# Performance work log

Measured on AMD Instinct MI355X. Metric: run time of the kernel, lower is better.

## Reference

```python
import jax, jax.numpy as jnp
import numpy as np

B, S, D = 4, 2048, 1024
LN_EPS = 1e-5
NEG_INF = -1e9


def _layernorm(x, gamma, beta):
    mu = jnp.mean(x, axis=-1, keepdims=True)
    var = jnp.var(x, axis=-1, keepdims=True)
    return (x - mu) * jax.lax.rsqrt(var + LN_EPS) * gamma + beta


def setup_inputs() -> dict:
    key = jax.random.key(0)
    k1, k2, k3, k4 = jax.random.split(key, 4)
    context = jax.random.normal(k1, (B, S, D), dtype=jnp.float32)
    eos_mask = jnp.ones((B, S, S), dtype=jnp.int64)
    prior = jax.random.uniform(k2, (B, S, S), dtype=jnp.float32)
    bound = 1.0 / np.sqrt(D)
    Wq = jax.random.uniform(k3, (D, D), dtype=jnp.float32, minval=-bound, maxval=bound)
    Wk = jax.random.uniform(k4, (D, D), dtype=jnp.float32, minval=-bound, maxval=bound)
    gamma = jnp.ones((D,), dtype=jnp.float32)
    beta = jnp.zeros((D,), dtype=jnp.float32)
    return {"context": context, "eos_mask": eos_mask, "prior": prior,
            "Wq": Wq, "Wk": Wk, "gamma": gamma, "beta": beta}


def reference(context, eos_mask, prior, Wq, Wk, gamma, beta):
    d_model = context.shape[-1]
    seq_len = context.shape[1]
    x = _layernorm(context, gamma, beta)
    q = x @ Wq.T                                   # nn.Linear, no bias
    k = x @ Wk.T
    scores = jnp.einsum('bsd,btd->bst', q, k) / jnp.sqrt(jnp.asarray(d_model, x.dtype))

    idx = jnp.arange(seq_len)
    a_sup = idx[:, None] + 1 == idx[None, :]       # superdiagonal (torch `a`)
    c_sub = idx[:, None] - 1 == idx[None, :]       # subdiagonal  (torch `c`)
    diag = idx[:, None] == idx[None, :]            # identity     (torch `b`)
    strict_lower = idx[:, None] > idx[None, :]     # tril - eye

    # mask = eos_mask & (a + c)  (Python precedence: & binds looser than +)
    mask = (eos_mask != 0) & (a_sup | c_sub)
    scores = jnp.where(mask, scores, NEG_INF)
    neibor_attn = jax.nn.softmax(scores, axis=-1)
    neibor_attn = jnp.sqrt(neibor_attn * jnp.swapaxes(neibor_attn, -1, -2) + 1e-9)
    neibor_attn = prior + (1.0 - prior) * neibor_attn

    # t = log(neibor+1e-9).masked_fill(a==0,0) @ tril  == reverse cumsum over last axis
    logn = jnp.where(a_sup, jnp.log(neibor_attn + 1e-9), 0.0)
    t = jnp.cumsum(logn[:, :, ::-1], axis=-1)[:, :, ::-1]
    # g = exp(tril @ t), keep strictly-lower part ((tril - eye) != 0)
    g = jnp.exp(jnp.cumsum(t, axis=1))
    g = jnp.where(strict_lower, g, 0.0)

    g_attn = g + jnp.swapaxes(g, -1, -2) + jnp.where(diag, neibor_attn, 1e-9)
    return g_attn, neibor_attn
```

## Files before the change

kernel.cpp:

```cpp
#include <hip/hip_runtime.h>
#include <hip/hip_bf16.h>
#include <stdint.h>

#define SS 2048
#define DD 1024
#define RR 8192

typedef _Float16 f16;
typedef _Float16 f16x8 __attribute__((ext_vector_type(8)));
typedef _Float16 f16x4 __attribute__((ext_vector_type(4)));
typedef float    f32x4 __attribute__((ext_vector_type(4)));

__device__ __forceinline__ void gl_lds16(const f16* g, f16* l) {
  __builtin_amdgcn_global_load_lds((const __attribute__((address_space(1))) void*)g,
                                   (__attribute__((address_space(3))) void*)l,
                                   16, 0, 0);
}

__global__ __launch_bounds__(256) void k_pre(const float* __restrict__ x,
                                             const float* __restrict__ gamma,
                                             const float* __restrict__ beta,
                                             f16* __restrict__ xn,
                                             const float* __restrict__ Wq,
                                             const float* __restrict__ Wk,
                                             f16* __restrict__ Wqt,
                                             f16* __restrict__ Wkt,
                                             const int* __restrict__ eos,
                                             const float* __restrict__ prior,
                                             float* __restrict__ sup_g,
                                             float* __restrict__ sub_g,
                                             int* __restrict__ e_sup,
                                             int* __restrict__ e_sub,
                                             float* __restrict__ pr_sup) {
  __shared__ f16 tile[64][72];
  int bidx = blockIdx.x;
  int t = threadIdx.x;
  if (bidx < RR) {
    int lane = t & 63, w = t >> 6;
    const float* xr = x + (size_t)bidx * DD;
    float4 v = ((const float4*)xr)[t];
    float s  = v.x + v.y + v.z + v.w;
    float ss = v.x*v.x + v.y*v.y + v.z*v.z + v.w*v.w;
#pragma unroll
    for (int off = 32; off > 0; off >>= 1) {
      s  += __shfl_down(s,  off, 64);
      ss += __shfl_down(ss, off, 64);
    }
    float* r0 = (float*)&tile[0][0];
    float* r1 = r0 + 4;
    if (lane == 0) { r0[w] = s; r1[w] = ss; }
    __syncthreads();
    float tot = r0[0]+r0[1]+r0[2]+r0[3];
    float tss = r1[0]+r1[1]+r1[2]+r1[3];
    float mu  = tot * (1.0f/DD);
    float var = tss * (1.0f/DD) - mu*mu;
    float inv = rsqrtf(var + 1e-5f);
    float4 g = ((const float4*)gamma)[t];
    float4 b = ((const float4*)beta)[t];
    f16x4 o;
    o[0] = (f16)((v.x-mu)*inv*g.x + b.x);
    o[1] = (f16)((v.y-mu)*inv*g.y + b.y);
    o[2] = (f16)((v.z-mu)*inv*g.z + b.z);
    o[3] = (f16)((v.w-mu)*inv*g.w + b.w);
    *(f16x4*)(xn + (size_t)bidx*DD + t*4) = o;
  } else if (bidx < RR + 512) {
    int bid = bidx - RR;
    const float* src = (bid & 1) ? Wk : Wq;
    f16* dst = (bid & 1) ? Wkt : Wqt;
    int tb = bid >> 1;
    int r0 = (tb >> 4) << 6, c0 = (tb & 15) << 6;
#pragma unroll
    for (int p = 0; p < 4; ++p) {
      int r = p * 16 + (t >> 4);
      int c = (t & 15) * 4;
      float4 v = *(const float4*)(src + (size_t)(r0 + r) * DD + c0 + c);
      tile[c + 0][r] = (f16)v.x; tile[c + 1][r] = (f16)v.y;
      tile[c + 2][r] = (f16)v.z; tile[c + 3][r] = (f16)v.w;
    }
    __syncthreads();
    int orow = t >> 2, och = (t & 3) * 16;
    f16x8 a = *(const f16x8*)&tile[orow][och];
    f16x8 b = *(const f16x8*)&tile[orow][och + 8];
    f16* o = dst + (size_t)(c0 + orow) * DD + r0 + och;
    *(f16x8*)o = a;
    *(f16x8*)(o + 8) = b;
  } else {
    int g = bidx - (RR + 512);
    int u = g * 256 + t;
    sup_g[u] = 0.f;
    sub_g[u] = 0.f;
    if (u < 4 * 2047) {
      int b = u / 2047;
      int s = u - b * 2047;
      size_t ebase = (size_t)b * SS * SS;
      int bS = b * SS;
      e_sup[bS + s]     = eos[ebase + (size_t)s * SS + s + 1];
      e_sub[bS + s + 1] = eos[ebase + (size_t)(s + 1) * SS + s];
      pr_sup[bS + s]    = prior[ebase + (size_t)s * SS + s + 1];
    }
  }
}

__global__ __launch_bounds__(256) void k_mgemm(const f16* __restrict__ A,
                                               const f16* __restrict__ Bw,
                                               f16* __restrict__ C) {
  constexpr int K = 1024;
  __shared__ f16 As[2][64 * 32];
  __shared__ f16 Bs[2][64 * 32];
  int cpx = (int)gridDim.x >> 3;
  int bid = ((int)blockIdx.x & 7) * cpx + ((int)blockIdx.x >> 3);
  int bm = bid >> 4, bn = bid & 15;
  int tid = threadIdx.x;
  int lane = tid & 63, w = tid >> 6;
  int wm = w >> 1, wn = w & 1;
  f32x4 acc[2][2] = {};

  int srow = w * 16 + (lane >> 2);
  int sch  = lane & 3;
  const f16* Ag = A  + (size_t)(bm * 64 + srow) * K + sch * 8;
  const f16* Bg = Bw + (size_t)(bn * 64 + srow) * K + sch * 8;
  f16* lA = &As[0][0] + w * 16 * 32;
  f16* lB = &Bs[0][0] + w * 16 * 32;
  int rlo = lane & 15, rch = (lane >> 4) * 8;

  gl_lds16(Ag, lA);
  gl_lds16(Bg, lB);
  for (int t = 0; t < 32; ++t) {
    int cur = t & 1;
    __syncthreads();
    if (t < 31) {
      gl_lds16(Ag + (t + 1) * 32, lA + (cur ^ 1) * 64 * 32);
      gl_lds16(Bg + (t + 1) * 32, lB + (cur ^ 1) * 64 * 32);
    }
    f16x8 af[2], bf[2];
#pragma unroll
    for (int mi = 0; mi < 2; ++mi)
      af[mi] = *(const f16x8*)(&As[cur][(wm * 32 + mi * 16 + rlo) * 32 + rch]);
#pragma unroll
    for (int ni = 0; ni < 2; ++ni)
      bf[ni] = *(const f16x8*)(&Bs[cur][(wn * 32 + ni * 16 + rlo) * 32 + rch]);
#pragma unroll
    for (int mi = 0; mi < 2; ++mi)
#pragma unroll
      for (int ni = 0; ni < 2; ++ni)
        acc[mi][ni] = __builtin_amdgcn_mfma_f32_16x16x32_f16(af[mi], bf[ni], acc[mi][ni], 0, 0, 0);
  }
  int c0 = (lane >> 4) * 4;
#pragma unroll
  for (int mi = 0; mi < 2; ++mi)
#pragma unroll
    for (int ni = 0; ni < 2; ++ni)
#pragma unroll
      for (int r = 0; r < 4; ++r) {
        int row = bm * 64 + wm * 32 + mi * 16 + c0 + r;
        int col = bn * 64 + wn * 32 + ni * 16 + rlo;
        C[(size_t)row * DD + col] = (f16)acc[mi][ni][r];
      }
}

__global__ __launch_bounds__(256) void k_ygemm(const f16* __restrict__ A,
                                               const f16* __restrict__ Bw,
                                               float* __restrict__ sup_g,
                                               float* __restrict__ sub_g) {
  constexpr int K = 1024, BM = 128, BN = 128;
  constexpr int XST = 136;
  __shared__ f16 As[BM * 32];
  __shared__ f16 Bs[BN * 32];
  __shared__ f16 Xs[130 * XST];
  int cpx = (int)gridDim.x >> 3;
  int bid = ((int)blockIdx.x & 7) * cpx + ((int)blockIdx.x >> 3);
  int bm = bid >> 3, bn = bid & 7;
  int tid = threadIdx.x;
  int lane = tid & 63, w = tid >> 6;
  int wm = w >> 1, wn = w & 1;

  f32x4 acc[4][4] = {};

  int srow = w * 16 + (lane >> 2);
  int sch  = lane & 3;
  const f16* Ag0 = A  + (size_t)(bm * BM + srow) * K + sch * 8;
  const f16* Ag1 = Ag0 + (size_t)64 * K;
  const f16* Bg0 = Bw + (size_t)(bn * BN + srow) * K + sch * 8;
  const f16* Bg1 = Bg0 + (size_t)64 * K;
  f16* lA0 = As + (w * 16) * 32;
  f16* lA1 = As + (64 + w * 16) * 32;
  f16* lB0 = Bs + (w * 16) * 32;
  f16* lB1 = Bs + (64 + w * 16) * 32;
  int rlo = lane & 15, rch = (lane >> 4) * 8;

  for (int kt = 0; kt < K; kt += 32) {
    __syncthreads();
    gl_lds16(Ag0 + kt, lA0);
    gl_lds16(Ag1 + kt, lA1);
    gl_lds16(Bg0 + kt, lB0);
    gl_lds16(Bg1 + kt, lB1);
    __syncthreads();
    f16x8 af[4], bf[4];
#pragma unroll
    for (int mi = 0; mi < 4; ++mi)
      af[mi] = *(const f16x8*)(As + (wm * 64 + mi * 16 + rlo) * 32 + rch);
#pragma unroll
    for (int ni = 0; ni < 4; ++ni)
      bf[ni] = *(const f16x8*)(Bs + (wn * 64 + ni * 16 + rlo) * 32 + rch);
#pragma unroll
    for (int mi = 0; mi < 4; ++mi)
#pragma unroll
      for (int ni = 0; ni < 4; ++ni)
        acc[mi][ni] = __builtin_amdgcn_mfma_f32_16x16x32_f16(af[mi], bf[ni], acc[mi][ni], 0, 0, 0);
  }
  int c0 = (lane >> 4) * 4;
  int slabBase = bm * BM - 1;
#pragma unroll
  for (int it = 0; it < 9; ++it) {
    int c = tid + it * 256;
    if (c < 130 * 16) {
      int rI = c >> 4, colc = (c & 15) * 8;
      int gr = slabBase + rI;
      gr = gr < 0 ? 0 : (gr > RR - 1 ? RR - 1 : gr);
      *(f16x8*)(Xs + rI * XST + colc) =
          *(const f16x8*)(A + (size_t)gr * K + bn * BN + colc);
    }
  }
  __syncthreads();
#pragma unroll
  for (int mi = 0; mi < 4; ++mi) {
#pragma unroll
    for (int r = 0; r < 4; ++r) {
      int rloc = wm * 64 + mi * 16 + c0 + r;
      float su = 0.f, sb = 0.f;
#pragma unroll
      for (int ni = 0; ni < 4; ++ni) {
        float y = acc[mi][ni][r];
        int colL = wn * 64 + ni * 16 + rlo;
        su += y * (float)Xs[rloc * XST + colL];
        sb += y * (float)Xs[(rloc + 2) * XST + colL];
      }
#pragma unroll
      for (int m = 1; m < 16; m <<= 1) {
        su += __shfl_xor(su, m, 64);
        sb += __shfl_xor(sb, m, 64);
      }
      if (rlo == 0) {
        int rho = bm * BM + rloc;
        if ((rho & (SS - 1)) != 0)
          atomicAdd(&sup_g[rho - 1], su * 0.03125f);
        if ((rho & (SS - 1)) != SS - 1)
          atomicAdd(&sub_g[rho + 1], sb * 0.03125f);
      }
    }
  }
}

__global__ __launch_bounds__(1024) void k_scan(const float* __restrict__ sup,
                                               const float* __restrict__ sub,
                                               const int* __restrict__ e_sup,
                                               const int* __restrict__ e_sub,
                                               const float* __restrict__ pr_sup,
                                               float* __restrict__ p_sup,
                                               float* __restrict__ p_sub,
                                               double* __restrict__ P) {
  int b = blockIdx.x, t = threadIdx.x;
  int lane = t & 63, wid = t >> 6;
  int bS = b * SS;
  __shared__ float  psub_sh[SS];
  __shared__ double wsum[16];
  float psup_loc[2];
#pragma unroll
  for (int e = 0; e < 2; ++e) {
    int s = 2*t + e;
    bool supOK = (s < SS-1) && (e_sup[bS + s] != 0);
    bool subOK = (s >= 1)   && (e_sub[bS + s] != 0);
    float ps = 0.f, pb = 0.f;
    if (supOK && subOK) {
      float Av = sup[bS + s], Cv = sub[bS + s];
      float m  = fmaxf(Av, Cv);
      float ea = expf(Av - m), eb = expf(Cv - m);
      float iv = 1.0f / (ea + eb);
      ps = ea * iv; pb = eb * iv;
    } else if (supOK) ps = 1.f;
    else if (subOK)   pb = 1.f;
    p_sup[bS + s] = ps; p_sub[bS + s] = pb;
    psub_sh[s] = pb; psup_loc[e] = ps;
  }
  __syncthreads();
  double L0 = 0.0, L1 = 0.0;
#pragma unroll
  for (int e = 0; e < 2; ++e) {
    int s = 2*t + e;
    double Lv = 0.0;
    if (s < SS-1) {
      float pr = pr_sup[bS + s];
      float vv = sqrtf(psup_loc[e] * psub_sh[s+1] + 1e-9f);
      Lv = (double)logf(pr + (1.f - pr)*vv + 1e-9f);
    }
    if (e == 0) L0 = Lv; else L1 = Lv;
  }
  double pairv = L0 + L1;
  double v = pairv;
#pragma unroll
  for (int off = 1; off < 64; off <<= 1) {
    double u = __shfl_up(v, off, 64);
    if (lane >= off) v += u;
  }
  if (lane == 63) wsum[wid] = v;
  __syncthreads();
  double base = 0.0;
  for (int wI = 0; wI < wid; ++wI) base += wsum[wI];
  double excl = base + v - pairv;
  P[bS + 2*t]     = excl + L0;
  P[bS + 2*t + 1] = excl + L0 + L1;
}

__global__ __launch_bounds__(256) void k_out(const float* __restrict__ prior,
                                             const float* __restrict__ p_sup,
                                             const float* __restrict__ p_sub,
                                             const double* __restrict__ P,
                                             float* __restrict__ g_out,
                                             float* __restrict__ n_out) {
  size_t v = (size_t)blockIdx.x * 256 + threadIdx.x;
  int j4   = (int)(v & 511);
  int rowg = (int)(v >> 9);
  int s = rowg & (SS - 1);
  int b = rowg >> 11;
  size_t base = (size_t)rowg * SS + j4 * 4;
  union F4 { float4 v4; float a[4]; };
  F4 prf; prf.v4 = *(const float4*)(prior + base);
  int bS = b * SS;
  double Ps  = P[bS + s];
  double Ps2 = (s >= 2) ? P[bS + s - 2] : 0.0;
  const float SQ9 = 3.1622776601683795e-5f;
  F4 gv, nv;
#pragma unroll
  for (int e = 0; e < 4; ++e) {
    int j = j4*4 + e;
    float pr = prf.a[e];
    float vv;
    if (j == s + 1)      vv = sqrtf(p_sup[bS+s] * p_sub[bS+s+1] + 1e-9f);
    else if (j == s - 1) vv = sqrtf(p_sub[bS+s] * p_sup[bS+s-1] + 1e-9f);
    else                 vv = SQ9;
    float na = pr + (1.f - pr) * vv;
    nv.a[e] = na;
    float g;
    if (s == j) g = na;
    else if (s > j) {
      double Pj2 = (j >= 2) ? P[bS + j - 2] : 0.0;
      g = expf((float)(Ps - Pj2)) + 1e-9f;
    } else {
      g = expf((float)(P[bS + j] - Ps2)) + 1e-9f;
    }
    gv.a[e] = g;
  }
  *(float4*)(g_out + base) = gv.v4;
  *(float4*)(n_out + base) = nv.v4;
}

extern "C" void kernel_launch(void* const* d_in, const int* in_sizes, int n_in,
                              void* d_out, int out_size, void* d_ws, size_t ws_size,
                              hipStream_t stream) {
  const float* context = (const float*)d_in[0];
  const int*   eos     = (const int*)d_in[1];
  const float* prior   = (const float*)d_in[2];
  const float* Wq      = (const float*)d_in[3];
  const float* Wk      = (const float*)d_in[4];
  const float* gamma   = (const float*)d_in[5];
  const float* beta    = (const float*)d_in[6];

  char* ws = (char*)d_ws;
  float*    sup    = (float*)(ws);
  float*    sub    = (float*)(ws + 32768);
  float*    p_sup  = (float*)(ws + 65536);
  float*    p_sub  = (float*)(ws + 98304);
  double*   P      = (double*)(ws + 131072);
  int*      e_sup  = (int*)(ws + 196608);
  int*      e_sub  = (int*)(ws + 229376);
  float*    pr_sup = (float*)(ws + 262144);
  const size_t smallEnd = 294912;

  const size_t XN_BYTES = (size_t)RR * DD * 2;
  const size_t WT_BYTES = (size_t)DD * DD * 2;
  const size_t bigNeed  = XN_BYTES + 3 * WT_BYTES;
  char* big;
  if (ws_size >= smallEnd + bigNeed) big = ws + smallEnd;
  else big = (char*)d_out + ((size_t)out_size * 4 - bigNeed);
  f16* Xn  = (f16*)big;
  f16* Wqt = (f16*)(big + XN_BYTES);
  f16* Wkt = (f16*)(big + XN_BYTES + WT_BYTES);
  f16* Mm  = (f16*)(big + XN_BYTES + 2 * WT_BYTES);

  k_pre<<<RR + 512 + 32, 256, 0, stream>>>(context, gamma, beta, Xn, Wq, Wk, Wqt, Wkt,
                                           eos, prior, sup, sub, e_sup, e_sub, pr_sup);
  k_mgemm<<<256, 256, 0, stream>>>(Wqt, Wkt, Mm);
  k_ygemm<<<512, 256, 0, stream>>>(Xn, Mm, sup, sub);
  k_scan<<<4, 1024, 0, stream>>>(sup, sub, e_sup, e_sub, pr_sup, p_sup, p_sub, P);
  float* g_out = (float*)d_out;
  float* n_out = g_out + (size_t)RR * SS;
  k_out<<<16384, 256, 0, stream>>>(prior, p_sup, p_sub, P, g_out, n_out);
}
```

Measured before the change: 111.5 us.

## Fuse Wq^T·Wk product into preprocessing kernel and shrink y-GEMM tiles

```diff
diff --git a/kernel.cpp b/kernel.cpp
--- a/kernel.cpp
+++ b/kernel.cpp
@@ -23,8 +23,7 @@
                                              f16* __restrict__ xn,
                                              const float* __restrict__ Wq,
                                              const float* __restrict__ Wk,
-                                             f16* __restrict__ Wqt,
-                                             f16* __restrict__ Wkt,
+                                             f16* __restrict__ Mm,
                                              const int* __restrict__ eos,
                                              const float* __restrict__ prior,
                                              float* __restrict__ sup_g,
@@ -32,12 +31,62 @@
                                              int* __restrict__ e_sup,
                                              int* __restrict__ e_sub,
                                              float* __restrict__ pr_sup) {
-  __shared__ f16 tile[64][72];
+  __shared__ f16 shmem[2 * 64 * 40];
   int bidx = blockIdx.x;
   int t = threadIdx.x;
-  if (bidx < RR) {
+  if (bidx < 256) {
+    int bi = bidx >> 4, bj = bidx & 15;
+    int i0 = bi * 64, j0 = bj * 64;
+    f16* Aq = shmem;
+    f16* Bk = shmem + 64 * 40;
     int lane = t & 63, w = t >> 6;
-    const float* xr = x + (size_t)bidx * DD;
+    int wm = w >> 1, wn = w & 1;
+    int rlo = lane & 15, rch = (lane >> 4) * 8;
+    int krow = t >> 4;
+    int cgrp = (t & 15) * 4;
+    f32x4 acc[2][2] = {};
+    for (int kk = 0; kk < DD; kk += 32) {
+      __syncthreads();
+#pragma unroll
+      for (int p = 0; p < 2; ++p) {
+        int kr = kk + p * 16 + krow;
+        float4 vq = *(const float4*)(Wq + (size_t)kr * DD + i0 + cgrp);
+        float4 vk = *(const float4*)(Wk + (size_t)kr * DD + j0 + cgrp);
+        int kl = p * 16 + krow;
+        Aq[(cgrp + 0) * 40 + kl] = (f16)vq.x; Aq[(cgrp + 1) * 40 + kl] = (f16)vq.y;
+        Aq[(cgrp + 2) * 40 + kl] = (f16)vq.z; Aq[(cgrp + 3) * 40 + kl] = (f16)vq.w;
+        Bk[(cgrp + 0) * 40 + kl] = (f16)vk.x; Bk[(cgrp + 1) * 40 + kl] = (f16)vk.y;
+        Bk[(cgrp + 2) * 40 + kl] = (f16)vk.z; Bk[(cgrp + 3) * 40 + kl] = (f16)vk.w;
+      }
+      __syncthreads();
+      f16x8 af[2], bf[2];
+#pragma unroll
+      for (int mi = 0; mi < 2; ++mi)
+        af[mi] = *(const f16x8*)(Aq + (wm * 32 + mi * 16 + rlo) * 40 + rch);
+#pragma unroll
+      for (int ni = 0; ni < 2; ++ni)
+        bf[ni] = *(const f16x8*)(Bk + (wn * 32 + ni * 16 + rlo) * 40 + rch);
+#pragma unroll
+      for (int mi = 0; mi < 2; ++mi)
+#pragma unroll
+        for (int ni = 0; ni < 2; ++ni)
+          acc[mi][ni] = __builtin_amdgcn_mfma_f32_16x16x32_f16(af[mi], bf[ni], acc[mi][ni], 0, 0, 0);
+    }
+    int c0 = (lane >> 4) * 4;
+#pragma unroll
+    for (int mi = 0; mi < 2; ++mi)
+#pragma unroll
+      for (int ni = 0; ni < 2; ++ni)
+#pragma unroll
+        for (int r = 0; r < 4; ++r) {
+          int row = i0 + wm * 32 + mi * 16 + c0 + r;
+          int col = j0 + wn * 32 + ni * 16 + rlo;
+          Mm[(size_t)row * DD + col] = (f16)acc[mi][ni][r];
+        }
+  } else if (bidx < 256 + RR) {
+    int row = bidx - 256;
+    int lane = t & 63, w = t >> 6;
+    const float* xr = x + (size_t)row * DD;
     float4 v = ((const float4*)xr)[t];
     float s  = v.x + v.y + v.z + v.w;
     float ss = v.x*v.x + v.y*v.y + v.z*v.z + v.w*v.w;
@@ -46,7 +95,7 @@
       s  += __shfl_down(s,  off, 64);
       ss += __shfl_down(ss, off, 64);
     }
-    float* r0 = (float*)&tile[0][0];
+    float* r0 = (float*)&shmem[0];
     float* r1 = r0 + 4;
     if (lane == 0) { r0[w] = s; r1[w] = ss; }
     __syncthreads();
@@ -62,30 +111,9 @@
     o[1] = (f16)((v.y-mu)*inv*g.y + b.y);
     o[2] = (f16)((v.z-mu)*inv*g.z + b.z);
     o[3] = (f16)((v.w-mu)*inv*g.w + b.w);
-    *(f16x4*)(xn + (size_t)bidx*DD + t*4) = o;
-  } else if (bidx < RR + 512) {
-    int bid = bidx - RR;
-    const float* src = (bid & 1) ? Wk : Wq;
-    f16* dst = (bid & 1) ? Wkt : Wqt;
-    int tb = bid >> 1;
-    int r0 = (tb >> 4) << 6, c0 = (tb & 15) << 6;
-#pragma unroll
-    for (int p = 0; p < 4; ++p) {
-      int r = p * 16 + (t >> 4);
-      int c = (t & 15) * 4;
-      float4 v = *(const float4*)(src + (size_t)(r0 + r) * DD + c0 + c);
-      tile[c + 0][r] = (f16)v.x; tile[c + 1][r] = (f16)v.y;
-      tile[c + 2][r] = (f16)v.z; tile[c + 3][r] = (f16)v.w;
-    }
-    __syncthreads();
-    int orow = t >> 2, och = (t & 3) * 16;
-    f16x8 a = *(const f16x8*)&tile[orow][och];
-    f16x8 b = *(const f16x8*)&tile[orow][och + 8];
-    f16* o = dst + (size_t)(c0 + orow) * DD + r0 + och;
-    *(f16x8*)o = a;
-    *(f16x8*)(o + 8) = b;
+    *(f16x4*)(xn + (size_t)row*DD + t*4) = o;
   } else {
-    int g = bidx - (RR + 512);
+    int g = bidx - (256 + RR);
     int u = g * 256 + t;
     sup_g[u] = 0.f;
     sub_g[u] = 0.f;
@@ -101,120 +129,62 @@
   }
 }
 
-__global__ __launch_bounds__(256) void k_mgemm(const f16* __restrict__ A,
+__global__ __launch_bounds__(256) void k_ygemm(const f16* __restrict__ A,
                                                const f16* __restrict__ Bw,
-                                               f16* __restrict__ C) {
-  constexpr int K = 1024;
-  __shared__ f16 As[2][64 * 32];
-  __shared__ f16 Bs[2][64 * 32];
+                                               float* __restrict__ sup_g,
+                                               float* __restrict__ sub_g) {
+  constexpr int K = 1024, BM = 128, BN = 64;
+  constexpr int XST = 72;
+  __shared__ f16 shmem[130 * XST];
+  f16* As = shmem;
+  f16* Bs = shmem + BM * 32;
+  f16* Xs = shmem;
   int cpx = (int)gridDim.x >> 3;
   int bid = ((int)blockIdx.x & 7) * cpx + ((int)blockIdx.x >> 3);
   int bm = bid >> 4, bn = bid & 15;
   int tid = threadIdx.x;
   int lane = tid & 63, w = tid >> 6;
   int wm = w >> 1, wn = w & 1;
-  f32x4 acc[2][2] = {};
-
-  int srow = w * 16 + (lane >> 2);
-  int sch  = lane & 3;
-  const f16* Ag = A  + (size_t)(bm * 64 + srow) * K + sch * 8;
-  const f16* Bg = Bw + (size_t)(bn * 64 + srow) * K + sch * 8;
-  f16* lA = &As[0][0] + w * 16 * 32;
-  f16* lB = &Bs[0][0] + w * 16 * 32;
-  int rlo = lane & 15, rch = (lane >> 4) * 8;
-
-  gl_lds16(Ag, lA);
-  gl_lds16(Bg, lB);
-  for (int t = 0; t < 32; ++t) {
-    int cur = t & 1;
-    __syncthreads();
-    if (t < 31) {
-      gl_lds16(Ag + (t + 1) * 32, lA + (cur ^ 1) * 64 * 32);
-      gl_lds16(Bg + (t + 1) * 32, lB + (cur ^ 1) * 64 * 32);
-    }
-    f16x8 af[2], bf[2];
-#pragma unroll
-    for (int mi = 0; mi < 2; ++mi)
-      af[mi] = *(const f16x8*)(&As[cur][(wm * 32 + mi * 16 + rlo) * 32 + rch]);
-#pragma unroll
-    for (int ni = 0; ni < 2; ++ni)
-      bf[ni] = *(const f16x8*)(&Bs[cur][(wn * 32 + ni * 16 + rlo) * 32 + rch]);
-#pragma unroll
-    for (int mi = 0; mi < 2; ++mi)
-#pragma unroll
-      for (int ni = 0; ni < 2; ++ni)
-        acc[mi][ni] = __builtin_amdgcn_mfma_f32_16x16x32_f16(af[mi], bf[ni], acc[mi][ni], 0, 0, 0);
-  }
-  int c0 = (lane >> 4) * 4;
-#pragma unroll
-  for (int mi = 0; mi < 2; ++mi)
-#pragma unroll
-    for (int ni = 0; ni < 2; ++ni)
-#pragma unroll
-      for (int r = 0; r < 4; ++r) {
-        int row = bm * 64 + wm * 32 + mi * 16 + c0 + r;
-        int col = bn * 64 + wn * 32 + ni * 16 + rlo;
-        C[(size_t)row * DD + col] = (f16)acc[mi][ni][r];
-      }
-}
-
-__global__ __launch_bounds__(256) void k_ygemm(const f16* __restrict__ A,
-                                               const f16* __restrict__ Bw,
-                                               float* __restrict__ sup_g,
-                                               float* __restrict__ sub_g) {
-  constexpr int K = 1024, BM = 128, BN = 128;
-  constexpr int XST = 136;
-  __shared__ f16 As[BM * 32];
-  __shared__ f16 Bs[BN * 32];
-  __shared__ f16 Xs[130 * XST];
-  int cpx = (int)gridDim.x >> 3;
-  int bid = ((int)blockIdx.x & 7) * cpx + ((int)blockIdx.x >> 3);
-  int bm = bid >> 3, bn = bid & 7;
-  int tid = threadIdx.x;
-  int lane = tid & 63, w = tid >> 6;
-  int wm = w >> 1, wn = w & 1;
-
-  f32x4 acc[4][4] = {};
+
+  f32x4 acc[4][2] = {};
 
   int srow = w * 16 + (lane >> 2);
   int sch  = lane & 3;
   const f16* Ag0 = A  + (size_t)(bm * BM + srow) * K + sch * 8;
   const f16* Ag1 = Ag0 + (size_t)64 * K;
-  const f16* Bg0 = Bw + (size_t)(bn * BN + srow) * K + sch * 8;
-  const f16* Bg1 = Bg0 + (size_t)64 * K;
+  const f16* Bg  = Bw + (size_t)(bn * BN + srow) * K + sch * 8;
   f16* lA0 = As + (w * 16) * 32;
   f16* lA1 = As + (64 + w * 16) * 32;
-  f16* lB0 = Bs + (w * 16) * 32;
-  f16* lB1 = Bs + (64 + w * 16) * 32;
+  f16* lB  = Bs + (w * 16) * 32;
   int rlo = lane & 15, rch = (lane >> 4) * 8;
 
   for (int kt = 0; kt < K; kt += 32) {
     __syncthreads();
     gl_lds16(Ag0 + kt, lA0);
     gl_lds16(Ag1 + kt, lA1);
-    gl_lds16(Bg0 + kt, lB0);
-    gl_lds16(Bg1 + kt, lB1);
+    gl_lds16(Bg  + kt, lB);
     __syncthreads();
-    f16x8 af[4], bf[4];
+    f16x8 af[4], bf[2];
 #pragma unroll
     for (int mi = 0; mi < 4; ++mi)
       af[mi] = *(const f16x8*)(As + (wm * 64 + mi * 16 + rlo) * 32 + rch);
 #pragma unroll
-    for (int ni = 0; ni < 4; ++ni)
-      bf[ni] = *(const f16x8*)(Bs + (wn * 64 + ni * 16 + rlo) * 32 + rch);
+    for (int ni = 0; ni < 2; ++ni)
+      bf[ni] = *(const f16x8*)(Bs + (wn * 32 + ni * 16 + rlo) * 32 + rch);
 #pragma unroll
     for (int mi = 0; mi < 4; ++mi)
 #pragma unroll
-      for (int ni = 0; ni < 4; ++ni)
+      for (int ni = 0; ni < 2; ++ni)
         acc[mi][ni] = __builtin_amdgcn_mfma_f32_16x16x32_f16(af[mi], bf[ni], acc[mi][ni], 0, 0, 0);
   }
   int c0 = (lane >> 4) * 4;
+  __syncthreads();
   int slabBase = bm * BM - 1;
 #pragma unroll
-  for (int it = 0; it < 9; ++it) {
+  for (int it = 0; it < 5; ++it) {
     int c = tid + it * 256;
-    if (c < 130 * 16) {
-      int rI = c >> 4, colc = (c & 15) * 8;
+    if (c < 130 * 8) {
+      int rI = c >> 3, colc = (c & 7) * 8;
       int gr = slabBase + rI;
       gr = gr < 0 ? 0 : (gr > RR - 1 ? RR - 1 : gr);
       *(f16x8*)(Xs + rI * XST + colc) =
@@ -229,9 +199,9 @@
       int rloc = wm * 64 + mi * 16 + c0 + r;
       float su = 0.f, sb = 0.f;
 #pragma unroll
-      for (int ni = 0; ni < 4; ++ni) {
+      for (int ni = 0; ni < 2; ++ni) {
         float y = acc[mi][ni][r];
-        int colL = wn * 64 + ni * 16 + rlo;
+        int colL = wn * 32 + ni * 16 + rlo;
         su += y * (float)Xs[rloc * XST + colL];
         sb += y * (float)Xs[(rloc + 2) * XST + colL];
       }
@@ -377,20 +347,17 @@
   const size_t smallEnd = 294912;
 
   const size_t XN_BYTES = (size_t)RR * DD * 2;
-  const size_t WT_BYTES = (size_t)DD * DD * 2;
-  const size_t bigNeed  = XN_BYTES + 3 * WT_BYTES;
+  const size_t M_BYTES  = (size_t)DD * DD * 2;
+  const size_t bigNeed  = XN_BYTES + M_BYTES;
   char* big;
   if (ws_size >= smallEnd + bigNeed) big = ws + smallEnd;
   else big = (char*)d_out + ((size_t)out_size * 4 - bigNeed);
-  f16* Xn  = (f16*)big;
-  f16* Wqt = (f16*)(big + XN_BYTES);
-  f16* Wkt = (f16*)(big + XN_BYTES + WT_BYTES);
-  f16* Mm  = (f16*)(big + XN_BYTES + 2 * WT_BYTES);
-
-  k_pre<<<RR + 512 + 32, 256, 0, stream>>>(context, gamma, beta, Xn, Wq, Wk, Wqt, Wkt,
+  f16* Xn = (f16*)big;
+  f16* Mm = (f16*)(big + XN_BYTES);
+
+  k_pre<<<256 + RR + 32, 256, 0, stream>>>(context, gamma, beta, Xn, Wq, Wk, Mm,
                                            eos, prior, sup, sub, e_sup, e_sub, pr_sup);
-  k_mgemm<<<256, 256, 0, stream>>>(Wqt, Wkt, Mm);
-  k_ygemm<<<512, 256, 0, stream>>>(Xn, Mm, sup, sub);
+  k_ygemm<<<1024, 256, 0, stream>>>(Xn, Mm, sup, sub);
   k_scan<<<4, 1024, 0, stream>>>(sup, sub, e_sup, e_sub, pr_sup, p_sup, p_sub, P);
   float* g_out = (float*)d_out;
   float* n_out = g_out + (size_t)RR * SS;
```

After: 138.1 us. 23.8% more time.
